# Kernel optimization log

Hardware: AMD Instinct MI355X
Metric: run time of the kernel (lower is better)

Reference implementation:

```python
import jax, jax.numpy as jnp
import numpy as np

B = 65536
H = 50          # hidden_size
L = 6           # num_layers
IN = 3          # input_size
T = 3           # seq_len


def setup_inputs() -> dict:
    key = jax.random.key(0)
    ks = jax.random.split(key, 10)
    s = 0.1  # weight init scale
    return {
        "x":     jax.random.normal(ks[0], (B, IN, T), dtype=jnp.float32),
        "h0":    jax.random.normal(ks[1], (L, B, H), dtype=jnp.float32),
        "c0":    jax.random.normal(ks[2], (L, B, H), dtype=jnp.float32),
        "w_ih0": jax.random.normal(ks[3], (4 * H, IN), dtype=jnp.float32) * s,
        "w_ih":  jax.random.normal(ks[4], (L - 1, 4 * H, H), dtype=jnp.float32) * s,
        "w_hh":  jax.random.normal(ks[5], (L, 4 * H, H), dtype=jnp.float32) * s,
        "b_ih":  jax.random.normal(ks[6], (L, 4 * H), dtype=jnp.float32) * s,
        "b_hh":  jax.random.normal(ks[7], (L, 4 * H), dtype=jnp.float32) * s,
        "fc_w":  jax.random.normal(ks[8], (1, H), dtype=jnp.float32) * s,
        "fc_b":  jax.random.normal(ks[9], (1,), dtype=jnp.float32) * s,
    }


def _lstm_layer(x_seq, h, c, w_ih, w_hh, b):
    """x_seq: [T, B, in]; returns all hidden states [T, B, H].
    PyTorch gate order: i, f, g, o."""
    def step(carry, x_t):
        h, c = carry
        gates = x_t @ w_ih.T + h @ w_hh.T + b  # [B, 4H]
        i, f, g, o = jnp.split(gates, 4, axis=-1)
        i = jax.nn.sigmoid(i)
        f = jax.nn.sigmoid(f)
        g = jnp.tanh(g)
        o = jax.nn.sigmoid(o)
        c = f * c + i * g
        h = o * jnp.tanh(c)
        return (h, c), h

    _, ys = jax.lax.scan(step, (h, c), x_seq)
    return ys


def reference(x, h0, c0, w_ih0, w_ih, w_hh, b_ih, b_hh, fc_w, fc_b):
    # original forward: input.permute(0, 2, 1) -> [B, T, IN], batch_first LSTM
    seq = jnp.transpose(x, (2, 0, 1))  # [T, B, IN] (time-major for scan)
    b = b_ih + b_hh                    # combined bias per layer [L, 4H]
    ys = _lstm_layer(seq, h0[0], c0[0], w_ih0, w_hh[0], b[0])
    for l in range(1, L):
        ys = _lstm_layer(ys, h0[l], c0[l], w_ih[l - 1], w_hh[l], b[l])
    # dropout(0.2) is identity in eval mode; take last timestep then fc
    last = ys[-1]                      # [B, H]
    return last @ fc_w.T + fc_b        # [B, 1]
```

## Files before the change

### kernel.cpp

```cpp
#include <hip/hip_runtime.h>


namespace {

constexpr int H  = 50;
constexpr int L  = 6;
constexpr int T  = 3;
constexpr int IN = 3;
constexpr int M  = 64;
constexpr int BLK = 1024;
constexpr int ROWS = 72;
constexpr int NSLOT = 5;

using half8  = __attribute__((ext_vector_type(8))) _Float16;
using half2v = __attribute__((ext_vector_type(2))) _Float16;
using f32x4  = __attribute__((ext_vector_type(4))) float;

__device__ __forceinline__ float rcp_(float x) { return __builtin_amdgcn_rcpf(x); }
__device__ __forceinline__ float ex2(float x)  { return __builtin_amdgcn_exp2f(x); }

__global__ void wprep(const float* __restrict__ w_ih0, const float* __restrict__ w_ihL,
                      const float* __restrict__ w_hh,  const float* __restrict__ b_ih,
                      const float* __restrict__ b_hh,  _Float16* __restrict__ wbuf) {
  int t = blockIdx.x * 256 + threadIdx.x;
  if (t >= 384 * 64) return;
  int lam = t & 63, f = t >> 6;
  int nt = f & 15, s = (f >> 4) & 3, l = f >> 6;
  int n = nt * 16 + (lam & 15);
  int j = n >> 2, gate = n & 3, row = gate * 50 + j;
  float scale = (gate == 2) ? 2.8853900817779268f : 1.4426950408889634f;
  _Float16 o8[8];
#pragma unroll
  for (int jj = 0; jj < 8; ++jj) {
    int k = s * 32 + (lam >> 4) * 8 + jj;
    float v = 0.f;
    if (j < H) {
      if (s < 2) {
        int ksz = (l == 0) ? IN : H;
        if (k < ksz) v = (l == 0) ? w_ih0[row * IN + k]
                                  : w_ihL[((size_t)(l - 1) * 200 + row) * H + k];
      } else {
        int kh = k - 64;
        if (kh < H)        v = w_hh[((size_t)l * 200 + row) * H + kh];
        else if (kh == 63) v = b_ih[l * 200 + row] + b_hh[l * 200 + row];
      }
    }
    o8[jj] = (_Float16)(v * scale);
  }
  ((half8*)wbuf)[t] = *(half8*)o8;
}

__global__ __launch_bounds__(BLK, 8)
void lstm_mfma(const float* __restrict__ x,   const float* __restrict__ h0,
               const float* __restrict__ c0,  const float* __restrict__ fc_w,
               const float* __restrict__ fc_b, const _Float16* __restrict__ wbuf,
               float* __restrict__ out, int B) {
  const int tid = threadIdx.x;
  const int lam = tid & 63;
  const int q   = lam >> 4;
  const int lm  = lam & 15;
  const int bbase = blockIdx.x * M;
  const int w   = __builtin_amdgcn_readfirstlane(tid >> 6);
  const int ntg = __builtin_amdgcn_readfirstlane((w + blockIdx.x) & 15);
  const bool live = (ntg <= 12);
  const int j = 4 * ntg + q;

  __shared__ __align__(16) _Float16 ys[NSLOT][M][ROWS];

  if (tid < NSLOT * M) {
    _Float16* row = &ys[0][0][0] + (size_t)tid * ROWS;
#pragma unroll
    for (int z = 0; z < 6; ++z)
      *(unsigned int*)(row + 50 + 2 * z) = 0u;
    half2v pb; pb[0] = (_Float16)0.f; pb[1] = (_Float16)1.f;
    *(half2v*)(row + 62) = pb;
  }
  if (tid < T * M) {
    const int t = tid >> 6, m = tid & 63;
    const float* xs = x + (size_t)(bbase + m) * (IN * T) + t;
    _Float16* row = &ys[2 + t][m][0];
    half2v p0; p0[0] = (_Float16)xs[0]; p0[1] = (_Float16)xs[3];
    half2v p1; p1[0] = (_Float16)xs[6]; p1[1] = (_Float16)0.f;
    *(half2v*)(row)     = p0;
    *(half2v*)(row + 2) = p1;
#pragma unroll
    for (int z = 0; z < 7; ++z)
      *(unsigned long long*)(row + 4 + 4 * z) = 0ull;
  }
  __syncthreads();

  float cc[4];
  f32x4 xa[4];
  half8 W4[4];
  const f32x4 z4 = {0.f, 0.f, 0.f, 0.f};
  int b = 0;

  for (int l = 0; l < L; ++l) {
    const int sh0 = b;
    int s1 = b + 1; if (s1 >= NSLOT) s1 -= NSLOT;
    int s2 = b + 2; if (s2 >= NSLOT) s2 -= NSLOT;
    int s3 = b + 3; if (s3 >= NSLOT) s3 -= NSLOT;
    int s4 = b + 4; if (s4 >= NSLOT) s4 -= NSLOT;

    if (live) {
#pragma unroll
      for (int mt = 0; mt < 4; ++mt)
        cc[mt] = (j < H)
            ? c0[((size_t)l * B + bbase + mt * 16 + lm) * H + j] : 0.f;
#pragma unroll
      for (int s = 0; s < 4; ++s)
        W4[s] = ((const half8*)wbuf)[((l * 4 + s) * 16 + ntg) * 64 + lam];
#pragma unroll
      for (int mt = 0; mt < 4; ++mt) {
        half8 X0 = *(const half8*)(&ys[s2][mt * 16 + lm][q * 8]);
        xa[mt] = __builtin_amdgcn_mfma_f32_16x16x32_f16(W4[0], X0, z4, 0, 0, 0);
      }
      if (l > 0) {
#pragma unroll
        for (int mt = 0; mt < 4; ++mt) {
          half8 X1 = *(const half8*)(&ys[s2][mt * 16 + lm][32 + q * 8]);
          xa[mt] = __builtin_amdgcn_mfma_f32_16x16x32_f16(W4[1], X1, xa[mt], 0, 0, 0);
        }
      }
    }
    {
      const int mg = tid >> 4, kpl = tid & 15;
      const float* hp = h0 + ((size_t)l * B + bbase + mg) * H + 2 * kpl;
      _Float16* dp = &ys[sh0][mg][2 * kpl];
      float2 v = *(const float2*)(hp);
      half2v pv; pv[0] = (_Float16)v.x; pv[1] = (_Float16)v.y;
      *(half2v*)dp = pv;
      if (kpl < 9) {
        float2 v2 = *(const float2*)(hp + 32);
        half2v p2; p2[0] = (_Float16)v2.x; p2[1] = (_Float16)v2.y;
        *(half2v*)(dp + 32) = p2;
      }
    }
    __syncthreads();

#pragma unroll
    for (int t = 0; t < T; ++t) {
      const int shs = (t == 0) ? sh0 : ((t == 1) ? s1 : s2);
      const int sot = (t == 0) ? s1  : ((t == 1) ? s2 : s3);
      const int sxt = (t == 0) ? s3  : s4;
      if (live) {
#pragma unroll
        for (int s = 0; s < 2; ++s)
#pragma unroll
          for (int mt = 0; mt < 4; ++mt) {
            half8 Hf = *(const half8*)(&ys[shs][mt * 16 + lm][s * 32 + q * 8]);
            xa[mt] = __builtin_amdgcn_mfma_f32_16x16x32_f16(W4[2 + s], Hf, xa[mt], 0, 0, 0);
          }
#pragma unroll
        for (int mt = 0; mt < 4; ++mt) {
          const float ig = rcp_(1.f + ex2(-xa[mt][0]));
          const float fg = rcp_(1.f + ex2(-xa[mt][1]));
          const float gg = 2.f * rcp_(1.f + ex2(-xa[mt][2])) - 1.f;
          const float og = rcp_(1.f + ex2(-xa[mt][3]));
          const float cv = fg * cc[mt] + ig * gg;
          cc[mt] = cv;
          const float tc = 2.f * rcp_(1.f + ex2(-2.8853900817779268f * cv)) - 1.f;
          if (j < H)
            ys[sot][mt * 16 + lm][j] = (_Float16)(og * tc);
        }
        if (t < T - 1) {
#pragma unroll
          for (int mt = 0; mt < 4; ++mt) {
            half8 X0 = *(const half8*)(&ys[sxt][mt * 16 + lm][q * 8]);
            xa[mt] = __builtin_amdgcn_mfma_f32_16x16x32_f16(W4[0], X0, z4, 0, 0, 0);
          }
          if (l > 0) {
#pragma unroll
            for (int mt = 0; mt < 4; ++mt) {
              half8 X1 = *(const half8*)(&ys[sxt][mt * 16 + lm][32 + q * 8]);
              xa[mt] = __builtin_amdgcn_mfma_f32_16x16x32_f16(W4[1], X1, xa[mt], 0, 0, 0);
            }
          }
        }
      }
      __syncthreads();
    }
    b = (b == 0) ? (NSLOT - 1) : b - 1;
  }

  if (tid < 512) {
    int m = tid >> 3, strip = tid & 7;
    float part = 0.f;
#pragma unroll
    for (int jj = 0; jj < 7; ++jj) {
      int jf = strip + 8 * jj;
      if (jf < H) part += fc_w[jf] * (float)ys[3][m][jf];
    }
    part += __shfl_xor(part, 4);
    part += __shfl_xor(part, 2);
    part += __shfl_xor(part, 1);
    if (strip == 0) out[bbase + m] = part + fc_b[0];
  }
}

}

extern "C" void kernel_launch(void* const* d_in, const int* in_sizes, int n_in,
                              void* d_out, int out_size, void* d_ws, size_t ws_size,
                              hipStream_t stream) {
  const float* x     = (const float*)d_in[0];
  const float* h0    = (const float*)d_in[1];
  const float* c0    = (const float*)d_in[2];
  const float* w_ih0 = (const float*)d_in[3];
  const float* w_ih  = (const float*)d_in[4];
  const float* w_hh  = (const float*)d_in[5];
  const float* b_ih  = (const float*)d_in[6];
  const float* b_hh  = (const float*)d_in[7];
  const float* fc_w  = (const float*)d_in[8];
  const float* fc_b  = (const float*)d_in[9];
  float* out         = (float*)d_out;

  const int B = in_sizes[0] / (IN * T);
  _Float16* wbuf = (_Float16*)d_ws;

  wprep<<<(384 * 64 + 255) / 256, 256, 0, stream>>>(w_ih0, w_ih, w_hh, b_ih, b_hh, wbuf);
  lstm_mfma<<<B / M, BLK, 0, stream>>>(x, h0, c0, fc_w, fc_b, wbuf, out, B);
}
```

Before: 268.1 us.

## Shrink batch tile to 16 rows, give each wave two gate tiles

Each block now handles 16 batch rows with 512 threads, and each of the 8 waves computes two N-tiles of gates, sharing one LDS B-fragment load across both MFMAs. The layer loop is fully unrolled, so slot indices are compile-time constants and the per-layer slot arithmetic goes away. The aim is more blocks, fewer idle waves (only one dead tile pair instead of three of sixteen waves), and less LDS traffic per MFMA. In exchange the weights are reloaded per block four times as often, and each wave holds more registers.

Result: slower. 279.2 us (+4.2%).

```diff
diff --git a/kernel.cpp b/kernel.cpp
--- a/kernel.cpp
+++ b/kernel.cpp
@@ -7,8 +7,8 @@
 constexpr int L  = 6;
 constexpr int T  = 3;
 constexpr int IN = 3;
-constexpr int M  = 64;
-constexpr int BLK = 1024;
+constexpr int M  = 16;
+constexpr int BLK = 512;
 constexpr int ROWS = 72;
 constexpr int NSLOT = 5;
 
@@ -60,10 +60,12 @@
   const int q   = lam >> 4;
   const int lm  = lam & 15;
   const int bbase = blockIdx.x * M;
-  const int w   = __builtin_amdgcn_readfirstlane(tid >> 6);
-  const int ntg = __builtin_amdgcn_readfirstlane((w + blockIdx.x) & 15);
-  const bool live = (ntg <= 12);
-  const int j = 4 * ntg + q;
+  const int ng  = __builtin_amdgcn_readfirstlane(tid >> 6);
+  const int ntp = __builtin_amdgcn_readfirstlane((ng + blockIdx.x) & 7);
+  const int ntg0 = 2 * ntp, ntg1 = 2 * ntp + 1;
+  const bool live0 = (ntg0 <= 12);
+  const bool live1 = (ntg1 <= 12);
+  const int j0 = 4 * ntg0 + q, j1 = 4 * ntg1 + q;
 
   __shared__ __align__(16) _Float16 ys[NSLOT][M][ROWS];
 
@@ -76,7 +78,7 @@
     *(half2v*)(row + 62) = pb;
   }
   if (tid < T * M) {
-    const int t = tid >> 6, m = tid & 63;
+    const int t = tid >> 4, m = tid & 15;
     const float* xs = x + (size_t)(bbase + m) * (IN * T) + t;
     _Float16* row = &ys[2 + t][m][0];
     half2v p0; p0[0] = (_Float16)xs[0]; p0[1] = (_Float16)xs[3];
@@ -89,51 +91,50 @@
   }
   __syncthreads();
 
-  float cc[4];
-  f32x4 xa[4];
-  half8 W4[4];
+  float cc[2];
+  f32x4 xa[2];
+  half8 W[2][4];
   const f32x4 z4 = {0.f, 0.f, 0.f, 0.f};
-  int b = 0;
-
+
+  const _Float16* rbase = &ys[0][lm][q * 8];
+
+#pragma unroll
   for (int l = 0; l < L; ++l) {
-    const int sh0 = b;
-    int s1 = b + 1; if (s1 >= NSLOT) s1 -= NSLOT;
-    int s2 = b + 2; if (s2 >= NSLOT) s2 -= NSLOT;
-    int s3 = b + 3; if (s3 >= NSLOT) s3 -= NSLOT;
-    int s4 = b + 4; if (s4 >= NSLOT) s4 -= NSLOT;
-
-    if (live) {
-#pragma unroll
-      for (int mt = 0; mt < 4; ++mt)
-        cc[mt] = (j < H)
-            ? c0[((size_t)l * B + bbase + mt * 16 + lm) * H + j] : 0.f;
+    const int sh0 = (4 * l) % 5;
+    const int s1 = (sh0 + 1) % 5;
+    const int s2 = (sh0 + 2) % 5;
+    const int s3 = (sh0 + 3) % 5;
+    const int s4 = (sh0 + 4) % 5;
+
+    if (live0) {
+      cc[0] = (j0 < H) ? c0[((size_t)l * B + bbase + lm) * H + j0] : 0.f;
+      cc[1] = (live1 && j1 < H) ? c0[((size_t)l * B + bbase + lm) * H + j1] : 0.f;
 #pragma unroll
       for (int s = 0; s < 4; ++s)
-        W4[s] = ((const half8*)wbuf)[((l * 4 + s) * 16 + ntg) * 64 + lam];
-#pragma unroll
-      for (int mt = 0; mt < 4; ++mt) {
-        half8 X0 = *(const half8*)(&ys[s2][mt * 16 + lm][q * 8]);
-        xa[mt] = __builtin_amdgcn_mfma_f32_16x16x32_f16(W4[0], X0, z4, 0, 0, 0);
-      }
-      if (l > 0) {
-#pragma unroll
-        for (int mt = 0; mt < 4; ++mt) {
-          half8 X1 = *(const half8*)(&ys[s2][mt * 16 + lm][32 + q * 8]);
-          xa[mt] = __builtin_amdgcn_mfma_f32_16x16x32_f16(W4[1], X1, xa[mt], 0, 0, 0);
+        W[0][s] = ((const half8*)wbuf)[((l * 4 + s) * 16 + ntg0) * 64 + lam];
+      if (live1)
+#pragma unroll
+        for (int s = 0; s < 4; ++s)
+          W[1][s] = ((const half8*)wbuf)[((l * 4 + s) * 16 + ntg1) * 64 + lam];
+      {
+        half8 Xf = *(const half8*)(rbase + s2 * (M * ROWS));
+        xa[0] = __builtin_amdgcn_mfma_f32_16x16x32_f16(W[0][0], Xf, z4, 0, 0, 0);
+        if (live1)
+          xa[1] = __builtin_amdgcn_mfma_f32_16x16x32_f16(W[1][0], Xf, z4, 0, 0, 0);
+        if (l > 0) {
+          half8 Xg = *(const half8*)(rbase + s2 * (M * ROWS) + 32);
+          xa[0] = __builtin_amdgcn_mfma_f32_16x16x32_f16(W[0][1], Xg, xa[0], 0, 0, 0);
+          if (live1)
+            xa[1] = __builtin_amdgcn_mfma_f32_16x16x32_f16(W[1][1], Xg, xa[1], 0, 0, 0);
         }
       }
     }
     {
-      const int mg = tid >> 4, kpl = tid & 15;
-      const float* hp = h0 + ((size_t)l * B + bbase + mg) * H + 2 * kpl;
-      _Float16* dp = &ys[sh0][mg][2 * kpl];
-      float2 v = *(const float2*)(hp);
-      half2v pv; pv[0] = (_Float16)v.x; pv[1] = (_Float16)v.y;
-      *(half2v*)dp = pv;
-      if (kpl < 9) {
-        float2 v2 = *(const float2*)(hp + 32);
-        half2v p2; p2[0] = (_Float16)v2.x; p2[1] = (_Float16)v2.y;
-        *(half2v*)(dp + 32) = p2;
+      const int mg = tid >> 5, kpl = tid & 31;
+      if (kpl < 25) {
+        float2 v = *(const float2*)(h0 + ((size_t)l * B + bbase + mg) * H + 2 * kpl);
+        half2v pv; pv[0] = (_Float16)v.x; pv[1] = (_Float16)v.y;
+        *(half2v*)(&ys[sh0][mg][2 * kpl]) = pv;
       }
     }
     __syncthreads();
@@ -143,47 +144,54 @@
       const int shs = (t == 0) ? sh0 : ((t == 1) ? s1 : s2);
       const int sot = (t == 0) ? s1  : ((t == 1) ? s2 : s3);
       const int sxt = (t == 0) ? s3  : s4;
-      if (live) {
-#pragma unroll
-        for (int s = 0; s < 2; ++s)
-#pragma unroll
-          for (int mt = 0; mt < 4; ++mt) {
-            half8 Hf = *(const half8*)(&ys[shs][mt * 16 + lm][s * 32 + q * 8]);
-            xa[mt] = __builtin_amdgcn_mfma_f32_16x16x32_f16(W4[2 + s], Hf, xa[mt], 0, 0, 0);
+      if (live0) {
+#pragma unroll
+        for (int s = 0; s < 2; ++s) {
+          half8 Hf = *(const half8*)(rbase + shs * (M * ROWS) + s * 32);
+          xa[0] = __builtin_amdgcn_mfma_f32_16x16x32_f16(W[0][2 + s], Hf, xa[0], 0, 0, 0);
+          if (live1)
+            xa[1] = __builtin_amdgcn_mfma_f32_16x16x32_f16(W[1][2 + s], Hf, xa[1], 0, 0, 0);
+        }
+        {
+          const float ig = rcp_(1.f + ex2(-xa[0][0]));
+          const float fg = rcp_(1.f + ex2(-xa[0][1]));
+          const float gg = 2.f * rcp_(1.f + ex2(-xa[0][2])) - 1.f;
+          const float og = rcp_(1.f + ex2(-xa[0][3]));
+          const float cv = fg * cc[0] + ig * gg;
+          cc[0] = cv;
+          const float tc = 2.f * rcp_(1.f + ex2(-2.8853900817779268f * cv)) - 1.f;
+          if (j0 < H)
+            ys[sot][lm][j0] = (_Float16)(og * tc);
+        }
+        if (live1) {
+          const float ig = rcp_(1.f + ex2(-xa[1][0]));
+          const float fg = rcp_(1.f + ex2(-xa[1][1]));
+          const float gg = 2.f * rcp_(1.f + ex2(-xa[1][2])) - 1.f;
+          const float og = rcp_(1.f + ex2(-xa[1][3]));
+          const float cv = fg * cc[1] + ig * gg;
+          cc[1] = cv;
+          const float tc = 2.f * rcp_(1.f + ex2(-2.8853900817779268f * cv)) - 1.f;
+          if (j1 < H)
+            ys[sot][lm][j1] = (_Float16)(og * tc);
+        }
+        if (t < T - 1) {
+          half8 Xf = *(const half8*)(rbase + sxt * (M * ROWS));
+          xa[0] = __builtin_amdgcn_mfma_f32_16x16x32_f16(W[0][0], Xf, z4, 0, 0, 0);
+          if (live1)
+            xa[1] = __builtin_amdgcn_mfma_f32_16x16x32_f16(W[1][0], Xf, z4, 0, 0, 0);
+          if (l > 0) {
+            half8 Xg = *(const half8*)(rbase + sxt * (M * ROWS) + 32);
+            xa[0] = __builtin_amdgcn_mfma_f32_16x16x32_f16(W[0][1], Xg, xa[0], 0, 0, 0);
+            if (live1)
+              xa[1] = __builtin_amdgcn_mfma_f32_16x16x32_f16(W[1][1], Xg, xa[1], 0, 0, 0);
           }
-#pragma unroll
-        for (int mt = 0; mt < 4; ++mt) {
-          const float ig = rcp_(1.f + ex2(-xa[mt][0]));
-          const float fg = rcp_(1.f + ex2(-xa[mt][1]));
-          const float gg = 2.f * rcp_(1.f + ex2(-xa[mt][2])) - 1.f;
-          const float og = rcp_(1.f + ex2(-xa[mt][3]));
-          const float cv = fg * cc[mt] + ig * gg;
-          cc[mt] = cv;
-          const float tc = 2.f * rcp_(1.f + ex2(-2.8853900817779268f * cv)) - 1.f;
-          if (j < H)
-            ys[sot][mt * 16 + lm][j] = (_Float16)(og * tc);
-        }
-        if (t < T - 1) {
-#pragma unroll
-          for (int mt = 0; mt < 4; ++mt) {
-            half8 X0 = *(const half8*)(&ys[sxt][mt * 16 + lm][q * 8]);
-            xa[mt] = __builtin_amdgcn_mfma_f32_16x16x32_f16(W4[0], X0, z4, 0, 0, 0);
-          }
-          if (l > 0) {
-#pragma unroll
-            for (int mt = 0; mt < 4; ++mt) {
-              half8 X1 = *(const half8*)(&ys[sxt][mt * 16 + lm][32 + q * 8]);
-              xa[mt] = __builtin_amdgcn_mfma_f32_16x16x32_f16(W4[1], X1, xa[mt], 0, 0, 0);
-            }
-          }
         }
       }
       __syncthreads();
     }
-    b = (b == 0) ? (NSLOT - 1) : b - 1;
-  }
-
-  if (tid < 512) {
+  }
+
+  if (tid < 8 * M) {
     int m = tid >> 3, strip = tid & 7;
     float part = 0.f;
 #pragma unroll
```

## Restructure LSTM kernel to single-wave blocks holding all gate tiles in registers

Applied to the files above, without the earlier changes.

Replaces the 1024-thread blocks, where each wave owned one 16-column gate tile for 64 batch rows, with 64-thread single-wave blocks of 32 batch rows. Each wave now loads all 13 tile weight fragments into registers and computes every gate tile itself. This removes all __syncthreads barriers and the three idle waves per block. The cost is much higher register pressure from the 52 half8 weight vectors plus 26 cell states, which lowers occupancy and risks spills. Each wave also reloads the whole layer's weights from cache.

After: 318.1 us. 1.19x slower.

```diff
diff --git a/kernel.cpp b/kernel.cpp
--- a/kernel.cpp
+++ b/kernel.cpp
@@ -7,10 +7,10 @@
 constexpr int L  = 6;
 constexpr int T  = 3;
 constexpr int IN = 3;
-constexpr int M  = 64;
-constexpr int BLK = 1024;
+constexpr int MW = 32;
 constexpr int ROWS = 72;
 constexpr int NSLOT = 5;
+constexpr int NT = 13;
 
 using half8  = __attribute__((ext_vector_type(8))) _Float16;
 using half2v = __attribute__((ext_vector_type(2))) _Float16;
@@ -50,33 +50,28 @@
   ((half8*)wbuf)[t] = *(half8*)o8;
 }
 
-__global__ __launch_bounds__(BLK, 8)
-void lstm_mfma(const float* __restrict__ x,   const float* __restrict__ h0,
+__global__ __launch_bounds__(64, 1)
+void lstm_wave(const float* __restrict__ x,   const float* __restrict__ h0,
                const float* __restrict__ c0,  const float* __restrict__ fc_w,
                const float* __restrict__ fc_b, const _Float16* __restrict__ wbuf,
                float* __restrict__ out, int B) {
-  const int tid = threadIdx.x;
-  const int lam = tid & 63;
+  const int lam = threadIdx.x;
   const int q   = lam >> 4;
   const int lm  = lam & 15;
-  const int bbase = blockIdx.x * M;
-  const int w   = __builtin_amdgcn_readfirstlane(tid >> 6);
-  const int ntg = __builtin_amdgcn_readfirstlane((w + blockIdx.x) & 15);
-  const bool live = (ntg <= 12);
-  const int j = 4 * ntg + q;
-
-  __shared__ __align__(16) _Float16 ys[NSLOT][M][ROWS];
-
-  if (tid < NSLOT * M) {
-    _Float16* row = &ys[0][0][0] + (size_t)tid * ROWS;
+  const int bbase = blockIdx.x * MW;
+
+  __shared__ __align__(16) _Float16 ys[NSLOT][MW][ROWS];
+
+  for (int r = lam; r < NSLOT * MW; r += 64) {
+    _Float16* row = &ys[0][0][0] + (size_t)r * ROWS;
 #pragma unroll
     for (int z = 0; z < 6; ++z)
       *(unsigned int*)(row + 50 + 2 * z) = 0u;
     half2v pb; pb[0] = (_Float16)0.f; pb[1] = (_Float16)1.f;
     *(half2v*)(row + 62) = pb;
   }
-  if (tid < T * M) {
-    const int t = tid >> 6, m = tid & 63;
+  for (int r = lam; r < T * MW; r += 64) {
+    const int t = r >> 5, m = r & 31;
     const float* xs = x + (size_t)(bbase + m) * (IN * T) + t;
     _Float16* row = &ys[2 + t][m][0];
     half2v p0; p0[0] = (_Float16)xs[0]; p0[1] = (_Float16)xs[3];
@@ -87,112 +82,94 @@
     for (int z = 0; z < 7; ++z)
       *(unsigned long long*)(row + 4 + 4 * z) = 0ull;
   }
-  __syncthreads();
-
-  float cc[4];
-  f32x4 xa[4];
-  half8 W4[4];
+
+  half8 W[NT][4];
+  float cc[2][NT];
   const f32x4 z4 = {0.f, 0.f, 0.f, 0.f};
-  int b = 0;
-
+
+  int sh0 = 0;
+#pragma unroll 1
   for (int l = 0; l < L; ++l) {
-    const int sh0 = b;
-    int s1 = b + 1; if (s1 >= NSLOT) s1 -= NSLOT;
-    int s2 = b + 2; if (s2 >= NSLOT) s2 -= NSLOT;
-    int s3 = b + 3; if (s3 >= NSLOT) s3 -= NSLOT;
-    int s4 = b + 4; if (s4 >= NSLOT) s4 -= NSLOT;
-
-    if (live) {
-#pragma unroll
-      for (int mt = 0; mt < 4; ++mt)
-        cc[mt] = (j < H)
+    const int p0 = sh0;
+    const int p1 = (sh0 + 1) % 5, p2 = (sh0 + 2) % 5;
+    const int p3 = (sh0 + 3) % 5, p4 = (sh0 + 4) % 5;
+
+#pragma unroll
+    for (int i = 0; i < NT; ++i)
+#pragma unroll
+      for (int s = 0; s < 4; ++s)
+        W[i][s] = ((const half8*)wbuf)[((l * 4 + s) * 16 + i) * 64 + lam];
+#pragma unroll
+    for (int mt = 0; mt < 2; ++mt)
+#pragma unroll
+      for (int i = 0; i < NT; ++i) {
+        const int j = 4 * i + q;
+        cc[mt][i] = (j < H)
             ? c0[((size_t)l * B + bbase + mt * 16 + lm) * H + j] : 0.f;
-#pragma unroll
-      for (int s = 0; s < 4; ++s)
-        W4[s] = ((const half8*)wbuf)[((l * 4 + s) * 16 + ntg) * 64 + lam];
-#pragma unroll
-      for (int mt = 0; mt < 4; ++mt) {
-        half8 X0 = *(const half8*)(&ys[s2][mt * 16 + lm][q * 8]);
-        xa[mt] = __builtin_amdgcn_mfma_f32_16x16x32_f16(W4[0], X0, z4, 0, 0, 0);
-      }
-      if (l > 0) {
-#pragma unroll
-        for (int mt = 0; mt < 4; ++mt) {
-          half8 X1 = *(const half8*)(&ys[s2][mt * 16 + lm][32 + q * 8]);
-          xa[mt] = __builtin_amdgcn_mfma_f32_16x16x32_f16(W4[1], X1, xa[mt], 0, 0, 0);
+      }
+    {
+      const int row = lam >> 1;
+      const int kp0 = (lam & 1) * 13;
+      const float* hp = h0 + ((size_t)l * B + bbase + row) * H;
+#pragma unroll
+      for (int p = 0; p < 13; ++p) {
+        const int kp = kp0 + p;
+        if (kp < 25) {
+          float2 v = *(const float2*)(hp + 2 * kp);
+          half2v pv; pv[0] = (_Float16)v.x; pv[1] = (_Float16)v.y;
+          *(half2v*)(&ys[p0][row][2 * kp]) = pv;
         }
       }
     }
-    {
-      const int mg = tid >> 4, kpl = tid & 15;
-      const float* hp = h0 + ((size_t)l * B + bbase + mg) * H + 2 * kpl;
-      _Float16* dp = &ys[sh0][mg][2 * kpl];
-      float2 v = *(const float2*)(hp);
-      half2v pv; pv[0] = (_Float16)v.x; pv[1] = (_Float16)v.y;
-      *(half2v*)dp = pv;
-      if (kpl < 9) {
-        float2 v2 = *(const float2*)(hp + 32);
-        half2v p2; p2[0] = (_Float16)v2.x; p2[1] = (_Float16)v2.y;
-        *(half2v*)(dp + 32) = p2;
-      }
-    }
-    __syncthreads();
 
 #pragma unroll
     for (int t = 0; t < T; ++t) {
-      const int shs = (t == 0) ? sh0 : ((t == 1) ? s1 : s2);
-      const int sot = (t == 0) ? s1  : ((t == 1) ? s2 : s3);
-      const int sxt = (t == 0) ? s3  : s4;
-      if (live) {
-#pragma unroll
-        for (int s = 0; s < 2; ++s)
-#pragma unroll
-          for (int mt = 0; mt < 4; ++mt) {
-            half8 Hf = *(const half8*)(&ys[shs][mt * 16 + lm][s * 32 + q * 8]);
-            xa[mt] = __builtin_amdgcn_mfma_f32_16x16x32_f16(W4[2 + s], Hf, xa[mt], 0, 0, 0);
-          }
-#pragma unroll
-        for (int mt = 0; mt < 4; ++mt) {
-          const float ig = rcp_(1.f + ex2(-xa[mt][0]));
-          const float fg = rcp_(1.f + ex2(-xa[mt][1]));
-          const float gg = 2.f * rcp_(1.f + ex2(-xa[mt][2])) - 1.f;
-          const float og = rcp_(1.f + ex2(-xa[mt][3]));
-          const float cv = fg * cc[mt] + ig * gg;
-          cc[mt] = cv;
+      const int shs = (t == 0) ? p0 : ((t == 1) ? p1 : p2);
+      const int sot = (t == 0) ? p1 : ((t == 1) ? p2 : p3);
+      const int sxt = (t == 0) ? p2 : ((t == 1) ? p3 : p4);
+
+      half8 X0[2], X1[2], Hf0[2], Hf1[2];
+#pragma unroll
+      for (int mt = 0; mt < 2; ++mt) {
+        const _Float16* xb = &ys[sxt][mt * 16 + lm][q * 8];
+        X0[mt] = *(const half8*)xb;
+        if (l > 0) X1[mt] = *(const half8*)(xb + 32);
+        const _Float16* hb = &ys[shs][mt * 16 + lm][q * 8];
+        Hf0[mt] = *(const half8*)hb;
+        Hf1[mt] = *(const half8*)(hb + 32);
+      }
+#pragma unroll
+      for (int mt = 0; mt < 2; ++mt)
+#pragma unroll
+        for (int i = 0; i < NT; ++i) {
+          f32x4 a = __builtin_amdgcn_mfma_f32_16x16x32_f16(W[i][0], X0[mt], z4, 0, 0, 0);
+          if (l > 0)
+            a = __builtin_amdgcn_mfma_f32_16x16x32_f16(W[i][1], X1[mt], a, 0, 0, 0);
+          a = __builtin_amdgcn_mfma_f32_16x16x32_f16(W[i][2], Hf0[mt], a, 0, 0, 0);
+          a = __builtin_amdgcn_mfma_f32_16x16x32_f16(W[i][3], Hf1[mt], a, 0, 0, 0);
+          const float ig = rcp_(1.f + ex2(-a[0]));
+          const float fg = rcp_(1.f + ex2(-a[1]));
+          const float gg = 2.f * rcp_(1.f + ex2(-a[2])) - 1.f;
+          const float og = rcp_(1.f + ex2(-a[3]));
+          const float cv = fg * cc[mt][i] + ig * gg;
+          cc[mt][i] = cv;
           const float tc = 2.f * rcp_(1.f + ex2(-2.8853900817779268f * cv)) - 1.f;
+          const int j = 4 * i + q;
           if (j < H)
             ys[sot][mt * 16 + lm][j] = (_Float16)(og * tc);
         }
-        if (t < T - 1) {
-#pragma unroll
-          for (int mt = 0; mt < 4; ++mt) {
-            half8 X0 = *(const half8*)(&ys[sxt][mt * 16 + lm][q * 8]);
-            xa[mt] = __builtin_amdgcn_mfma_f32_16x16x32_f16(W4[0], X0, z4, 0, 0, 0);
-          }
-          if (l > 0) {
-#pragma unroll
-            for (int mt = 0; mt < 4; ++mt) {
-              half8 X1 = *(const half8*)(&ys[sxt][mt * 16 + lm][32 + q * 8]);
-              xa[mt] = __builtin_amdgcn_mfma_f32_16x16x32_f16(W4[1], X1, xa[mt], 0, 0, 0);
-            }
-          }
-        }
-      }
-      __syncthreads();
-    }
-    b = (b == 0) ? (NSLOT - 1) : b - 1;
-  }
-
-  if (tid < 512) {
-    int m = tid >> 3, strip = tid & 7;
+    }
+    sh0 = (sh0 == 0) ? 4 : sh0 - 1;
+  }
+
+  {
+    const int m = lam >> 1, strip = lam & 1;
     float part = 0.f;
 #pragma unroll
-    for (int jj = 0; jj < 7; ++jj) {
-      int jf = strip + 8 * jj;
-      if (jf < H) part += fc_w[jf] * (float)ys[3][m][jf];
-    }
-    part += __shfl_xor(part, 4);
-    part += __shfl_xor(part, 2);
+    for (int jj = 0; jj < 25; ++jj) {
+      const int jf = 2 * jj + strip;
+      part += fc_w[jf] * (float)ys[3][m][jf];
+    }
     part += __shfl_xor(part, 1);
     if (strip == 0) out[bbase + m] = part + fc_b[0];
   }
@@ -219,5 +196,5 @@
   _Float16* wbuf = (_Float16*)d_ws;
 
   wprep<<<(384 * 64 + 255) / 256, 256, 0, stream>>>(w_ih0, w_ih, w_hh, b_ih, b_hh, wbuf);
-  lstm_mfma<<<B / M, BLK, 0, stream>>>(x, h0, c0, fc_w, fc_b, wbuf, out, B);
-}
+  lstm_wave<<<B / MW, 64, 0, stream>>>(x, h0, c0, fc_w, fc_b, wbuf, out, B);
+}
```

## Prefetch next layer's h0 into the free slot and fuse gate math into fewer reciprocals

Applied to the files above, without the earlier changes.

Moves the per-layer h0 staging out of the layer prologue: layer 0's h0 is loaded during initial setup, and each later layer's h0 is written into the free ring slot during the previous layer's last timestep. This removes one __syncthreads per layer. The gate activation math is also restructured algebraically so that the sigmoid and tanh terms share reciprocals, taking two rcp per element instead of six. The fused form multiplies several (1+exp) terms together, which risks overflow or inf/NaN for large pre-activations.

After: 252.5 us. 5.8% less time.

```diff
diff --git a/kernel.cpp b/kernel.cpp
--- a/kernel.cpp
+++ b/kernel.cpp
@@ -87,6 +87,19 @@
     for (int z = 0; z < 7; ++z)
       *(unsigned long long*)(row + 4 + 4 * z) = 0ull;
   }
+  {
+    const int mg = tid >> 4, kpl = tid & 15;
+    const float* hp = h0 + ((size_t)bbase + mg) * H + 2 * kpl;
+    _Float16* dp = &ys[0][mg][2 * kpl];
+    float2 v = *(const float2*)(hp);
+    half2v pv; pv[0] = (_Float16)v.x; pv[1] = (_Float16)v.y;
+    *(half2v*)dp = pv;
+    if (kpl < 9) {
+      float2 v2 = *(const float2*)(hp + 32);
+      half2v p2; p2[0] = (_Float16)v2.x; p2[1] = (_Float16)v2.y;
+      *(half2v*)(dp + 32) = p2;
+    }
+  }
   __syncthreads();
 
   float cc[4];
@@ -94,6 +107,23 @@
   half8 W4[4];
   const f32x4 z4 = {0.f, 0.f, 0.f, 0.f};
   int b = 0;
+
+#define ACT1(mt, sot_) do {                                                    \
+    const float zi = ex2(-xa[mt][0]);                                          \
+    const float zf = ex2(-xa[mt][1]);                                          \
+    const float zg = ex2(-xa[mt][2]);                                          \
+    const float zo = ex2(-xa[mt][3]);                                          \
+    const float pi_ = 1.f + zi, pf_ = 1.f + zf, pg_ = 1.f + zg, po_ = 1.f + zo;\
+    const float t1 = pi_ * pg_;                                                \
+    const float r1 = rcp_(t1 * pf_);                                           \
+    const float cv = (cc[mt] * t1 + (1.f - zg) * pf_) * r1;                    \
+    cc[mt] = cv;                                                               \
+    const float zc = ex2(-2.8853900817779268f * cv);                           \
+    const float pc_ = 1.f + zc;                                                \
+    const float hv = (1.f - zc) * rcp_(pc_ * po_);                             \
+    if (j < H)                                 \
+      ys[sot_][(mt) * 16 + lm][j] = (_Float16)hv;                              \
+  } while (0)
 
   for (int l = 0; l < L; ++l) {
     const int sh0 = b;
@@ -123,20 +153,6 @@
         }
       }
     }
-    {
-      const int mg = tid >> 4, kpl = tid & 15;
-      const float* hp = h0 + ((size_t)l * B + bbase + mg) * H + 2 * kpl;
-      _Float16* dp = &ys[sh0][mg][2 * kpl];
-      float2 v = *(const float2*)(hp);
-      half2v pv; pv[0] = (_Float16)v.x; pv[1] = (_Float16)v.y;
-      *(half2v*)dp = pv;
-      if (kpl < 9) {
-        float2 v2 = *(const float2*)(hp + 32);
-        half2v p2; p2[0] = (_Float16)v2.x; p2[1] = (_Float16)v2.y;
-        *(half2v*)(dp + 32) = p2;
-      }
-    }
-    __syncthreads();
 
 #pragma unroll
     for (int t = 0; t < T; ++t) {
@@ -151,18 +167,7 @@
             half8 Hf = *(const half8*)(&ys[shs][mt * 16 + lm][s * 32 + q * 8]);
             xa[mt] = __builtin_amdgcn_mfma_f32_16x16x32_f16(W4[2 + s], Hf, xa[mt], 0, 0, 0);
           }
-#pragma unroll
-        for (int mt = 0; mt < 4; ++mt) {
-          const float ig = rcp_(1.f + ex2(-xa[mt][0]));
-          const float fg = rcp_(1.f + ex2(-xa[mt][1]));
-          const float gg = 2.f * rcp_(1.f + ex2(-xa[mt][2])) - 1.f;
-          const float og = rcp_(1.f + ex2(-xa[mt][3]));
-          const float cv = fg * cc[mt] + ig * gg;
-          cc[mt] = cv;
-          const float tc = 2.f * rcp_(1.f + ex2(-2.8853900817779268f * cv)) - 1.f;
-          if (j < H)
-            ys[sot][mt * 16 + lm][j] = (_Float16)(og * tc);
-        }
+        ACT1(0, sot); ACT1(1, sot); ACT1(2, sot); ACT1(3, sot);
         if (t < T - 1) {
 #pragma unroll
           for (int mt = 0; mt < 4; ++mt) {
@@ -178,10 +183,24 @@
           }
         }
       }
+      if (t == T - 1 && l < L - 1) {
+        const int mg = tid >> 4, kpl = tid & 15;
+        const float* hp = h0 + (((size_t)l + 1) * B + bbase + mg) * H + 2 * kpl;
+        _Float16* dp = &ys[s4][mg][2 * kpl];
+        float2 v = *(const float2*)(hp);
+        half2v pv; pv[0] = (_Float16)v.x; pv[1] = (_Float16)v.y;
+        *(half2v*)dp = pv;
+        if (kpl < 9) {
+          float2 v2 = *(const float2*)(hp + 32);
+          half2v p2; p2[0] = (_Float16)v2.x; p2[1] = (_Float16)v2.y;
+          *(half2v*)(dp + 32) = p2;
+        }
+      }
       __syncthreads();
     }
     b = (b == 0) ? (NSLOT - 1) : b - 1;
   }
+#undef ACT1
 
   if (tid < 512) {
     int m = tid >> 3, strip = tid & 7;
```
